# Optimization experiments

Measured on AMD Instinct MI355X. Metric: run time of the kernel, lower is better.

The kernel has to match this reference:

```python
import jax, jax.numpy as jnp
import numpy as np

B, S, D, H, L, FF, V = 2, 1024, 1024, 16, 4, 2048, 32000
DK = D // H
EPS = 1e-5  # torch LayerNorm default


def _pos_enc(n, d):
    # matches torch PositionalEncoding: pe[pos, 2i]=sin, pe[pos, 2i+1]=cos
    pos = jnp.arange(n, dtype=jnp.float32)[:, None]
    div = jnp.exp(jnp.arange(0, d, 2, dtype=jnp.float32) * (-jnp.log(10000.0) / d))
    pe = jnp.zeros((n, d), dtype=jnp.float32)
    pe = pe.at[:, 0::2].set(jnp.sin(pos * div))
    pe = pe.at[:, 1::2].set(jnp.cos(pos * div))
    return pe


def setup_inputs() -> dict:
    key = jax.random.key(0)
    ks = jax.random.split(key, 12)
    s = 0.02
    return {
        "tokens": jax.random.randint(ks[0], (B, S), 0, V, dtype=jnp.int32),
        "emb": jax.random.normal(ks[1], (V, D), jnp.float32) * s,
        "Wq": jax.random.normal(ks[2], (L, D, D), jnp.float32) * s,
        "bq": jnp.zeros((L, D), jnp.float32),
        "Wk": jax.random.normal(ks[3], (L, D, D), jnp.float32) * s,
        "bk": jnp.zeros((L, D), jnp.float32),
        "Wv": jax.random.normal(ks[4], (L, D, D), jnp.float32) * s,
        "bv": jnp.zeros((L, D), jnp.float32),
        "Wo": jax.random.normal(ks[5], (L, D, D), jnp.float32) * s,
        "bo": jnp.zeros((L, D), jnp.float32),
        "W1": jax.random.normal(ks[6], (L, D, FF), jnp.float32) * s,
        "b1": jnp.zeros((L, FF), jnp.float32),
        "W2": jax.random.normal(ks[7], (L, FF, D), jnp.float32) * s,
        "b2": jnp.zeros((L, D), jnp.float32),
        "gamma": jnp.ones((L, D), jnp.float32),
        "beta": jnp.zeros((L, D), jnp.float32),
    }


def _layernorm(x, g, b):
    mu = jnp.mean(x, axis=-1, keepdims=True)
    var = jnp.mean(jnp.square(x - mu), axis=-1, keepdims=True)
    return (x - mu) * jax.lax.rsqrt(var + EPS) * g + b


def _encoder_layer(x, p):
    Wq, bq, Wk, bk, Wv, bv, Wo, bo, W1, b1, W2, b2, g, be = p
    # naive MHA: explicit QK^T / softmax / AV, materializing [B,H,S,S]
    q = (x @ Wq + bq).reshape(B, S, H, DK).transpose(0, 2, 1, 3)
    k = (x @ Wk + bk).reshape(B, S, H, DK).transpose(0, 2, 1, 3)
    v = (x @ Wv + bv).reshape(B, S, H, DK).transpose(0, 2, 1, 3)
    scores = jnp.einsum("bhqd,bhkd->bhqk", q, k) / jnp.sqrt(jnp.float32(DK))
    attn = jax.nn.softmax(scores, axis=-1)
    o = jnp.einsum("bhqk,bhkd->bhqd", attn, v)
    o = o.transpose(0, 2, 1, 3).reshape(B, S, D) @ Wo + bo
    # NOTE: same LayerNorm params used twice, as in the original module
    x = _layernorm(x + o, g, be)
    f = jax.nn.relu(x @ W1 + b1) @ W2 + b2
    x = _layernorm(x + f, g, be)
    return x, None


def reference(tokens, emb, Wq, bq, Wk, bk, Wv, bv, Wo, bo, W1, b1, W2, b2, gamma, beta):
    x = emb[tokens]  # [B,S,D]
    # faithful to the original bug: pe[:x.size(0)] indexes the BATCH dim,
    # pe slice has shape [B,1,D] and broadcasts over the sequence dim
    x = x + _pos_enc(B, D)[:, None, :]
    params = (Wq, bq, Wk, bk, Wv, bv, Wo, bo, W1, b1, W2, b2, gamma, beta)
    x, _ = jax.lax.scan(_encoder_layer, x, params)
    return x
```

## Files before the change

### kernel.cpp

```cpp
#include <hip/hip_runtime.h>
#include <cstdint>
#include <cstddef>

#define Bx 2
#define Sx 1024
#define Dx 1024
#define Hx 16
#define Lx 4
#define FFx 2048
#define DKx 64
#define Mx (Bx * Sx)

typedef __attribute__((ext_vector_type(4))) float f32x4;
typedef __attribute__((ext_vector_type(8))) __bf16 bf16x8;

__global__ void embed_kernel(const int* __restrict__ tokens,
                             const float* __restrict__ emb,
                             float* __restrict__ x, __bf16* __restrict__ xb) {
  size_t i = (size_t)blockIdx.x * blockDim.x + threadIdx.x;
  if (i >= (size_t)Mx * Dx) return;
  int d = (int)(i % Dx);
  size_t bs = i / Dx;
  int b = (int)(bs / Sx);
  int tok = tokens[bs];
  int dd = d & ~1;
  float arg = (float)b * expf((float)dd * (-logf(10000.0f) / (float)Dx));
  float pe = (d & 1) ? cosf(arg) : sinf(arg);
  float v = emb[(size_t)tok * Dx + d] + pe;
  x[i] = v;
  xb[i] = (__bf16)v;
}

__global__ void transpose_to_bf16(const float* __restrict__ W, __bf16* __restrict__ Wt,
                                  int K, int N, size_t sstride, size_t dstride) {
  __shared__ float tile[32][33];
  const float* Ws = W + blockIdx.z * sstride;
  __bf16* Wd = Wt + blockIdx.z * dstride;
  int tx = threadIdx.x, ty = threadIdx.y;
  int n0 = blockIdx.x * 32, k0 = blockIdx.y * 32;
#pragma unroll
  for (int i = 0; i < 4; ++i)
    tile[ty + 8 * i][tx] = Ws[(size_t)(k0 + ty + 8 * i) * N + n0 + tx];
  __syncthreads();
#pragma unroll
  for (int i = 0; i < 4; ++i)
    Wd[(size_t)(n0 + ty + 8 * i) * K + k0 + tx] = (__bf16)tile[tx][ty + 8 * i];
}

__global__ void concat3_kernel(const float* __restrict__ a, const float* __restrict__ b,
                               const float* __restrict__ c, float* __restrict__ out) {
  int i = blockIdx.x * 256 + threadIdx.x;
  int l = i / 3072, j = i % 3072;
  float v = (j < 1024) ? a[l * 1024 + j]
                       : ((j < 2048) ? b[l * 1024 + j - 1024] : c[l * 1024 + j - 2048]);
  out[i] = v;
}

__global__ void transpose_v(const __bf16* __restrict__ qkvb, __bf16* __restrict__ Vt) {
  __shared__ __bf16 tile[32][40];
  int s0 = blockIdx.x * 32;
  int d0 = (blockIdx.y & 1) * 32;
  int h = blockIdx.y >> 1, b = blockIdx.z;
  int tx = threadIdx.x, ty = threadIdx.y;
  const __bf16* src = qkvb + ((size_t)b * Sx + s0) * 3072 + 2048 + h * 64 + d0;
#pragma unroll
  for (int i = 0; i < 4; ++i)
    tile[ty + 8 * i][tx] = src[(size_t)(ty + 8 * i) * 3072 + tx];
  __syncthreads();
  __bf16* dst = Vt + ((size_t)(b * Hx + h) * 64 + d0) * Sx + s0;
#pragma unroll
  for (int i = 0; i < 4; ++i)
    dst[(size_t)(ty + 8 * i) * Sx + tx] = tile[tx][ty + 8 * i];
}

__device__ __forceinline__ void gld_lds16(const void* g, void* l) {
  __builtin_amdgcn_global_load_lds(
      (const __attribute__((address_space(1))) void*)(uintptr_t)g,
      (__attribute__((address_space(3))) void*)(uintptr_t)l, 16, 0, 0);
}

template <int TM, int TN, bool RELU, typename OutT>
__global__ __launch_bounds__(256) void gemm_bt(const __bf16* __restrict__ A,
                                               const __bf16* __restrict__ Bt,
                                               const float* __restrict__ bias,
                                               OutT* __restrict__ C0,
                                               float* __restrict__ C1,
                                               int Kstep, int Kld, int ldc) {
  static_assert((TM + TN) == 192, "NCH fixed at 12");
  __shared__ __align__(16) __bf16 lds[(TM + TN) * 32];
  const int t = threadIdx.x;
  const int w = t >> 6, lane = t & 63;
  const int quad = lane >> 4, l16 = lane & 15;
  const int m0 = blockIdx.y * TM, n0 = blockIdx.x * TN;
  const int lr = lane >> 2, lc = (lane & 3) * 8;
  const int koff = blockIdx.z * Kstep;

  f32x4 acc[2][4] = {};

  const int WR = (TN == 128) ? (w >> 1) * (TM / 2) : w * (TM / 4);
  const int WC = (TN == 128) ? (w & 1) * 64 : 0;
  const __bf16* Abase = A + (size_t)m0 * Kld + koff;
  const __bf16* Bbase = Bt + (size_t)n0 * Kld + koff;

  for (int k0 = 0; k0 < Kstep; k0 += 32) {
    __syncthreads();
#pragma unroll
    for (int c = 0; c < 3; ++c) {
      const int ch = c * 4 + w;
      const int r = ch * 16 + lr;
      const __bf16* g = (r < TM) ? (Abase + (size_t)r * Kld + k0 + lc)
                                 : (Bbase + (size_t)(r - TM) * Kld + k0 + lc);
      gld_lds16(g, (void*)(lds + ch * 512));
    }
    __syncthreads();
    bf16x8 af[2], bfr[4];
#pragma unroll
    for (int i = 0; i < 2; ++i)
      af[i] = *(const bf16x8*)&lds[(WR + i * 16 + l16) * 32 + quad * 8];
#pragma unroll
    for (int j = 0; j < 4; ++j)
      bfr[j] = *(const bf16x8*)&lds[(TM + WC + j * 16 + l16) * 32 + quad * 8];
#pragma unroll
    for (int i = 0; i < 2; ++i)
#pragma unroll
      for (int j = 0; j < 4; ++j)
        acc[i][j] = __builtin_amdgcn_mfma_f32_16x16x32_bf16(af[i], bfr[j], acc[i][j], 0, 0, 0);
  }

  const bool z0 = (blockIdx.z == 0);
  const int col0 = n0 + WC + l16;
#pragma unroll
  for (int j = 0; j < 4; ++j) {
    const int n = col0 + j * 16;
    const float bn = z0 ? bias[n] : 0.f;
#pragma unroll
    for (int i = 0; i < 2; ++i) {
#pragma unroll
      for (int r = 0; r < 4; ++r) {
        const int m = m0 + WR + i * 16 + quad * 4 + r;
        float v = acc[i][j][r] + bn;
        if (RELU) v = fmaxf(v, 0.f);
        if (z0)
          C0[(size_t)m * ldc + n] = (OutT)v;
        else
          C1[(size_t)m * ldc + n] = v;
      }
    }
  }
}

__global__ __launch_bounds__(256) void attention_mfma(const __bf16* __restrict__ QKV,
                                                      const __bf16* __restrict__ Vt,
                                                      __bf16* __restrict__ O) {
  __shared__ __align__(16) __bf16 Ks[2][64 * 72];
  __shared__ __align__(16) __bf16 Vs[2][64 * 72];
  __shared__ __align__(16) __bf16 Pl[64 * 72];

  const int t = threadIdx.x;
  const int w = t >> 6, lane = t & 63;
  const int quad = lane >> 4, l16 = lane & 15;
  const int q0 = blockIdx.x * 64;
  const int h = blockIdx.y, b = blockIdx.z;
  const size_t rowbase = (size_t)b * Sx;
  const int hoff = h * 64;

  const __bf16* qrow = QKV + (rowbase + q0 + w * 16 + l16) * 3072 + hoff;
  bf16x8 qf0 = *(const bf16x8*)(qrow + quad * 8);
  bf16x8 qf1 = *(const bf16x8*)(qrow + 32 + quad * 8);

  const __bf16* Kbase = QKV + rowbase * 3072 + 1024 + hoff;
  const __bf16* Vbase = Vt + (size_t)(b * Hx + h) * 64 * Sx;

  const int srow = t >> 2, sseg = t & 3;
  bf16x8 kp0, kp1, vp0, vp1;

  f32x4 oacc[4] = {};
  f32x4 lacc = {0.f, 0.f, 0.f, 0.f};
  const float cs = 0.125f * 1.44269504089f;

  {
    const __bf16* kr = Kbase + (size_t)srow * 3072 + sseg * 16;
    kp0 = *(const bf16x8*)kr;
    kp1 = *(const bf16x8*)(kr + 8);
    const __bf16* vr = Vbase + (size_t)srow * Sx + sseg * 16;
    vp0 = *(const bf16x8*)vr;
    vp1 = *(const bf16x8*)(vr + 8);
    *(bf16x8*)&Ks[0][srow * 72 + sseg * 16] = kp0;
    *(bf16x8*)&Ks[0][srow * 72 + sseg * 16 + 8] = kp1;
    *(bf16x8*)&Vs[0][srow * 72 + sseg * 16] = vp0;
    *(bf16x8*)&Vs[0][srow * 72 + sseg * 16 + 8] = vp1;
  }
  __syncthreads();

  for (int kt = 0; kt < Sx / 64; ++kt) {
    const int cur = kt & 1;
    if (kt < Sx / 64 - 1) {
      const int kn = (kt + 1) * 64;
      const __bf16* kr = Kbase + (size_t)(kn + srow) * 3072 + sseg * 16;
      kp0 = *(const bf16x8*)kr;
      kp1 = *(const bf16x8*)(kr + 8);
      const __bf16* vr = Vbase + (size_t)srow * Sx + kn + sseg * 16;
      vp0 = *(const bf16x8*)vr;
      vp1 = *(const bf16x8*)(vr + 8);
    }

    f32x4 s[4] = {};
#pragma unroll
    for (int j = 0; j < 4; ++j) {
      bf16x8 b0 = *(const bf16x8*)&Ks[cur][(j * 16 + l16) * 72 + quad * 8];
      bf16x8 b1 = *(const bf16x8*)&Ks[cur][(j * 16 + l16) * 72 + 32 + quad * 8];
      s[j] = __builtin_amdgcn_mfma_f32_16x16x32_bf16(qf0, b0, s[j], 0, 0, 0);
      s[j] = __builtin_amdgcn_mfma_f32_16x16x32_bf16(qf1, b1, s[j], 0, 0, 0);
    }

#pragma unroll
    for (int j = 0; j < 4; ++j) {
#pragma unroll
      for (int r = 0; r < 4; ++r) s[j][r] = __builtin_exp2f(s[j][r] * cs);
      lacc += s[j];
    }

#pragma unroll
    for (int r = 0; r < 4; ++r) {
      const int prow = (w * 16 + quad * 4 + r) * 72;
#pragma unroll
      for (int j = 0; j < 4; ++j) Pl[prow + j * 16 + l16] = (__bf16)s[j][r];
    }
    bf16x8 pa0 = *(const bf16x8*)&Pl[(w * 16 + l16) * 72 + quad * 8];
    bf16x8 pa1 = *(const bf16x8*)&Pl[(w * 16 + l16) * 72 + 32 + quad * 8];

#pragma unroll
    for (int j = 0; j < 4; ++j) {
      bf16x8 vb0 = *(const bf16x8*)&Vs[cur][(j * 16 + l16) * 72 + quad * 8];
      bf16x8 vb1 = *(const bf16x8*)&Vs[cur][(j * 16 + l16) * 72 + 32 + quad * 8];
      oacc[j] = __builtin_amdgcn_mfma_f32_16x16x32_bf16(pa0, vb0, oacc[j], 0, 0, 0);
      oacc[j] = __builtin_amdgcn_mfma_f32_16x16x32_bf16(pa1, vb1, oacc[j], 0, 0, 0);
    }

    if (kt < Sx / 64 - 1) {
      const int nxt = 1 - cur;
      *(bf16x8*)&Ks[nxt][srow * 72 + sseg * 16] = kp0;
      *(bf16x8*)&Ks[nxt][srow * 72 + sseg * 16 + 8] = kp1;
      *(bf16x8*)&Vs[nxt][srow * 72 + sseg * 16] = vp0;
      *(bf16x8*)&Vs[nxt][srow * 72 + sseg * 16 + 8] = vp1;
    }
    __syncthreads();
  }

#pragma unroll
  for (int r = 0; r < 4; ++r) {
    float lr = lacc[r];
    lr += __shfl_xor(lr, 1);
    lr += __shfl_xor(lr, 2);
    lr += __shfl_xor(lr, 4);
    lr += __shfl_xor(lr, 8);
    const float inv = 1.f / lr;
    const size_t orow = (rowbase + q0 + w * 16 + quad * 4 + r) * 1024 + hoff;
#pragma unroll
    for (int j = 0; j < 4; ++j) O[orow + j * 16 + l16] = (__bf16)(oacc[j][r] * inv);
  }
}

__global__ void add_ln_kernel(const float* __restrict__ x, const float* __restrict__ r0,
                              const float* __restrict__ r1,
                              const float* __restrict__ gamma, const float* __restrict__ beta,
                              float* __restrict__ out, __bf16* __restrict__ outb) {
  int row = blockIdx.x, t = threadIdx.x;
  __shared__ float red[256];
  const float* xr = x + (size_t)row * Dx;
  const float* rr0 = r0 + (size_t)row * Dx;
  const float* rr1 = r1 + (size_t)row * Dx;
  float v[4];
  float s = 0.f;
#pragma unroll
  for (int i = 0; i < 4; ++i) {
    int c = t + i * 256;
    v[i] = xr[c] + rr0[c] + rr1[c];
    s += v[i];
  }
  red[t] = s;
  __syncthreads();
  for (int off = 128; off > 0; off >>= 1) {
    if (t < off) red[t] += red[t + off];
    __syncthreads();
  }
  float mu = red[0] * (1.f / Dx);
  __syncthreads();
  float vs = 0.f;
#pragma unroll
  for (int i = 0; i < 4; ++i) {
    float d = v[i] - mu;
    vs += d * d;
  }
  red[t] = vs;
  __syncthreads();
  for (int off = 128; off > 0; off >>= 1) {
    if (t < off) red[t] += red[t + off];
    __syncthreads();
  }
  float is = rsqrtf(red[0] * (1.f / Dx) + 1e-5f);
  float* orow = out + (size_t)row * Dx;
  __bf16* brow = outb + (size_t)row * Dx;
#pragma unroll
  for (int i = 0; i < 4; ++i) {
    int c = t + i * 256;
    float y = (v[i] - mu) * is * gamma[c] + beta[c];
    orow[c] = y;
    brow[c] = (__bf16)y;
  }
}

extern "C" void kernel_launch(void* const* d_in, const int* in_sizes, int n_in,
                              void* d_out, int out_size, void* d_ws, size_t ws_size,
                              hipStream_t stream) {
  const int* tokens = (const int*)d_in[0];
  const float* emb = (const float*)d_in[1];
  const float* Wq = (const float*)d_in[2];
  const float* bq = (const float*)d_in[3];
  const float* Wk = (const float*)d_in[4];
  const float* bk = (const float*)d_in[5];
  const float* Wv = (const float*)d_in[6];
  const float* bv = (const float*)d_in[7];
  const float* Wo = (const float*)d_in[8];
  const float* bo = (const float*)d_in[9];
  const float* W1 = (const float*)d_in[10];
  const float* b1 = (const float*)d_in[11];
  const float* W2 = (const float*)d_in[12];
  const float* b2 = (const float*)d_in[13];
  const float* gamma = (const float*)d_in[14];
  const float* beta = (const float*)d_in[15];

  const size_t M1 = 1024 * 1024;
  float* ws = (float*)d_ws;
  float* x = ws;
  float* tmp = ws + 2 * M1;
  __bf16* bfr = (__bf16*)(ws + 4 * M1);
  __bf16* xb = bfr;
  __bf16* qkvb = bfr + 2 * M1;
  __bf16* ob = bfr + 8 * M1;
  __bf16* h1b = bfr + 10 * M1;
  __bf16* Vt = bfr + 14 * M1;
  __bf16* WqkvT = bfr + 16 * M1;
  __bf16* WoT = bfr + 28 * M1;
  __bf16* W1T = bfr + 32 * M1;
  __bf16* W2T = bfr + 40 * M1;
  float* bqkv = (float*)(bfr + 48 * M1);
  float* tmp1 = (float*)qkvb;

  embed_kernel<<<((size_t)Mx * Dx + 255) / 256, 256, 0, stream>>>(tokens, emb, x, xb);

  dim3 tb(32, 8);
  transpose_to_bf16<<<dim3(32, 32, Lx), tb, 0, stream>>>(Wq, WqkvT, Dx, Dx, M1, 3 * M1);
  transpose_to_bf16<<<dim3(32, 32, Lx), tb, 0, stream>>>(Wk, WqkvT + M1, Dx, Dx, M1, 3 * M1);
  transpose_to_bf16<<<dim3(32, 32, Lx), tb, 0, stream>>>(Wv, WqkvT + 2 * M1, Dx, Dx, M1, 3 * M1);
  transpose_to_bf16<<<dim3(32, 32, Lx), tb, 0, stream>>>(Wo, WoT, Dx, Dx, M1, M1);
  transpose_to_bf16<<<dim3(64, 32, Lx), tb, 0, stream>>>(W1, W1T, Dx, FFx, 2 * M1, 2 * M1);
  transpose_to_bf16<<<dim3(32, 64, Lx), tb, 0, stream>>>(W2, W2T, FFx, Dx, 2 * M1, 2 * M1);
  concat3_kernel<<<Lx * 12, 256, 0, stream>>>(bq, bk, bv, bqkv);

  for (int l = 0; l < Lx; ++l) {
    const __bf16* WqkvT_l = WqkvT + (size_t)l * 3 * M1;
    const __bf16* WoT_l = WoT + (size_t)l * M1;
    const __bf16* W1T_l = W1T + (size_t)l * 2 * M1;
    const __bf16* W2T_l = W2T + (size_t)l * 2 * M1;
    const float* bqkv_l = bqkv + (size_t)l * 3072;
    const float* bo_l = bo + (size_t)l * Dx;
    const float* b1_l = b1 + (size_t)l * FFx;
    const float* b2_l = b2 + (size_t)l * Dx;
    const float* g_l = gamma + (size_t)l * Dx;
    const float* be_l = beta + (size_t)l * Dx;

    gemm_bt<128, 64, false, __bf16><<<dim3(3072 / 64, Mx / 128, 1), 256, 0, stream>>>(
        xb, WqkvT_l, bqkv_l, qkvb, nullptr, Dx, Dx, 3072);

    transpose_v<<<dim3(32, 32, Bx), tb, 0, stream>>>(qkvb, Vt);
    attention_mfma<<<dim3(Sx / 64, Hx, Bx), 256, 0, stream>>>(qkvb, Vt, ob);

    gemm_bt<64, 128, false, float><<<dim3(Dx / 128, Mx / 64, 2), 256, 0, stream>>>(
        ob, WoT_l, bo_l, tmp, tmp1, Dx / 2, Dx, Dx);
    add_ln_kernel<<<Mx, 256, 0, stream>>>(x, tmp, tmp1, g_l, be_l, x, xb);

    gemm_bt<128, 64, true, __bf16><<<dim3(FFx / 64, Mx / 128, 1), 256, 0, stream>>>(
        xb, W1T_l, b1_l, h1b, nullptr, Dx, Dx, FFx);
    gemm_bt<64, 128, false, float><<<dim3(Dx / 128, Mx / 64, 2), 256, 0, stream>>>(
        h1b, W2T_l, b2_l, tmp, tmp1, FFx / 2, FFx, Dx);
    add_ln_kernel<<<Mx, 256, 0, stream>>>(x, tmp, tmp1, g_l, be_l,
                                          (l == Lx - 1) ? (float*)d_out : x, xb);
  }
}
```

Before: 821.1 us.

## Fuse V transpose into QKV GEMM epilogue and vectorize LayerNorm and embedding

The QKV GEMM epilogue now writes the V columns straight into the transposed Vt layout, so the separate transpose_v kernel and its extra read and write of V are gone. The add+LayerNorm kernel is rewritten to use float4 vector loads and stores with wavefront shuffle reductions in place of a shared-memory tree that needed many barriers. The embedding kernel handles element pairs with one sincos call and float2 accesses. The V epilogue now does narrower, strided bf16x4 stores and skips writing V into qkvb, which relies on attention reading V only from Vt.

```diff
diff --git a/kernel.cpp b/kernel.cpp
--- a/kernel.cpp
+++ b/kernel.cpp
@@ -13,22 +13,30 @@
 
 typedef __attribute__((ext_vector_type(4))) float f32x4;
 typedef __attribute__((ext_vector_type(8))) __bf16 bf16x8;
+typedef __attribute__((ext_vector_type(4))) __bf16 bf16x4;
+typedef __attribute__((ext_vector_type(2))) __bf16 bf16x2;
 
 __global__ void embed_kernel(const int* __restrict__ tokens,
                              const float* __restrict__ emb,
                              float* __restrict__ x, __bf16* __restrict__ xb) {
   size_t i = (size_t)blockIdx.x * blockDim.x + threadIdx.x;
-  if (i >= (size_t)Mx * Dx) return;
-  int d = (int)(i % Dx);
-  size_t bs = i / Dx;
-  int b = (int)(bs / Sx);
+  if (i >= (size_t)Mx * Dx / 2) return;
+  int p = (int)(i % (Dx / 2));
+  size_t bs = i / (Dx / 2);
+  int b = (int)(bs >> 10);
   int tok = tokens[bs];
-  int dd = d & ~1;
-  float arg = (float)b * expf((float)dd * (-logf(10000.0f) / (float)Dx));
-  float pe = (d & 1) ? cosf(arg) : sinf(arg);
-  float v = emb[(size_t)tok * Dx + d] + pe;
-  x[i] = v;
-  xb[i] = (__bf16)v;
+  float arg = (float)b * expf((float)(2 * p) * (-logf(10000.0f) / (float)Dx));
+  float sv, cv;
+  __sincosf(arg, &sv, &cv);
+  const float2 e = ((const float2*)(emb + (size_t)tok * Dx))[p];
+  float2 o;
+  o.x = e.x + sv;
+  o.y = e.y + cv;
+  ((float2*)x)[i] = o;
+  bf16x2 ob;
+  ob[0] = (__bf16)o.x;
+  ob[1] = (__bf16)o.y;
+  ((bf16x2*)xb)[i] = ob;
 }
 
 __global__ void transpose_to_bf16(const float* __restrict__ W, __bf16* __restrict__ Wt,
@@ -56,35 +64,19 @@
   out[i] = v;
 }
 
-__global__ void transpose_v(const __bf16* __restrict__ qkvb, __bf16* __restrict__ Vt) {
-  __shared__ __bf16 tile[32][40];
-  int s0 = blockIdx.x * 32;
-  int d0 = (blockIdx.y & 1) * 32;
-  int h = blockIdx.y >> 1, b = blockIdx.z;
-  int tx = threadIdx.x, ty = threadIdx.y;
-  const __bf16* src = qkvb + ((size_t)b * Sx + s0) * 3072 + 2048 + h * 64 + d0;
-#pragma unroll
-  for (int i = 0; i < 4; ++i)
-    tile[ty + 8 * i][tx] = src[(size_t)(ty + 8 * i) * 3072 + tx];
-  __syncthreads();
-  __bf16* dst = Vt + ((size_t)(b * Hx + h) * 64 + d0) * Sx + s0;
-#pragma unroll
-  for (int i = 0; i < 4; ++i)
-    dst[(size_t)(ty + 8 * i) * Sx + tx] = tile[tx][ty + 8 * i];
-}
-
 __device__ __forceinline__ void gld_lds16(const void* g, void* l) {
   __builtin_amdgcn_global_load_lds(
       (const __attribute__((address_space(1))) void*)(uintptr_t)g,
       (__attribute__((address_space(3))) void*)(uintptr_t)l, 16, 0, 0);
 }
 
-template <int TM, int TN, bool RELU, typename OutT>
+template <int TM, int TN, bool RELU, typename OutT, bool VOUT = false>
 __global__ __launch_bounds__(256) void gemm_bt(const __bf16* __restrict__ A,
                                                const __bf16* __restrict__ Bt,
                                                const float* __restrict__ bias,
                                                OutT* __restrict__ C0,
                                                float* __restrict__ C1,
+                                               __bf16* __restrict__ VT,
                                                int Kstep, int Kld, int ldc) {
   static_assert((TM + TN) == 192, "NCH fixed at 12");
   __shared__ __align__(16) __bf16 lds[(TM + TN) * 32];
@@ -127,8 +119,29 @@
         acc[i][j] = __builtin_amdgcn_mfma_f32_16x16x32_bf16(af[i], bfr[j], acc[i][j], 0, 0, 0);
   }
 
+  const int col0 = n0 + WC + l16;
+
+  if (VOUT && n0 >= 2048) {
+    const int b = m0 >> 10;
+    const int sbase = (m0 & 1023) + WR;
+#pragma unroll
+    for (int j = 0; j < 4; ++j) {
+      const int n = col0 + j * 16;
+      const int dk = n - 2048;
+      const float bn = bias[n];
+      __bf16* vrow = VT + (size_t)(b * 1024 + dk) * Sx + sbase;
+#pragma unroll
+      for (int i = 0; i < 2; ++i) {
+        bf16x4 pk;
+#pragma unroll
+        for (int r = 0; r < 4; ++r) pk[r] = (__bf16)(acc[i][j][r] + bn);
+        *(bf16x4*)(vrow + i * 16 + quad * 4) = pk;
+      }
+    }
+    return;
+  }
+
   const bool z0 = (blockIdx.z == 0);
-  const int col0 = n0 + WC + l16;
 #pragma unroll
   for (int j = 0; j < 4; ++j) {
     const int n = col0 + j * 16;
@@ -265,49 +278,34 @@
                               const float* __restrict__ r1,
                               const float* __restrict__ gamma, const float* __restrict__ beta,
                               float* __restrict__ out, __bf16* __restrict__ outb) {
-  int row = blockIdx.x, t = threadIdx.x;
-  __shared__ float red[256];
-  const float* xr = x + (size_t)row * Dx;
-  const float* rr0 = r0 + (size_t)row * Dx;
-  const float* rr1 = r1 + (size_t)row * Dx;
-  float v[4];
-  float s = 0.f;
-#pragma unroll
-  for (int i = 0; i < 4; ++i) {
-    int c = t + i * 256;
-    v[i] = xr[c] + rr0[c] + rr1[c];
-    s += v[i];
-  }
-  red[t] = s;
+  const int row = blockIdx.x, t = threadIdx.x;
+  const int lane = t & 63, w = t >> 6;
+  __shared__ float red[2][4];
+  const f32x4* xr = (const f32x4*)(x + (size_t)row * Dx);
+  const f32x4* a0 = (const f32x4*)(r0 + (size_t)row * Dx);
+  const f32x4* a1 = (const f32x4*)(r1 + (size_t)row * Dx);
+  f32x4 v = xr[t] + a0[t] + a1[t];
+  float s = v[0] + v[1] + v[2] + v[3];
+#pragma unroll
+  for (int off = 1; off < 64; off <<= 1) s += __shfl_xor(s, off);
+  if (lane == 0) red[0][w] = s;
   __syncthreads();
-  for (int off = 128; off > 0; off >>= 1) {
-    if (t < off) red[t] += red[t + off];
-    __syncthreads();
-  }
-  float mu = red[0] * (1.f / Dx);
+  const float mu = (red[0][0] + red[0][1] + red[0][2] + red[0][3]) * (1.f / Dx);
+  f32x4 d = v - mu;
+  float vs = d[0] * d[0] + d[1] * d[1] + d[2] * d[2] + d[3] * d[3];
+#pragma unroll
+  for (int off = 1; off < 64; off <<= 1) vs += __shfl_xor(vs, off);
+  if (lane == 0) red[1][w] = vs;
   __syncthreads();
-  float vs = 0.f;
-#pragma unroll
-  for (int i = 0; i < 4; ++i) {
-    float d = v[i] - mu;
-    vs += d * d;
-  }
-  red[t] = vs;
-  __syncthreads();
-  for (int off = 128; off > 0; off >>= 1) {
-    if (t < off) red[t] += red[t + off];
-    __syncthreads();
-  }
-  float is = rsqrtf(red[0] * (1.f / Dx) + 1e-5f);
-  float* orow = out + (size_t)row * Dx;
-  __bf16* brow = outb + (size_t)row * Dx;
-#pragma unroll
-  for (int i = 0; i < 4; ++i) {
-    int c = t + i * 256;
-    float y = (v[i] - mu) * is * gamma[c] + beta[c];
-    orow[c] = y;
-    brow[c] = (__bf16)y;
-  }
+  const float is = rsqrtf((red[1][0] + red[1][1] + red[1][2] + red[1][3]) * (1.f / Dx) + 1e-5f);
+  f32x4 g = ((const f32x4*)gamma)[t];
+  f32x4 be = ((const f32x4*)beta)[t];
+  f32x4 y = d * is * g + be;
+  ((f32x4*)(out + (size_t)row * Dx))[t] = y;
+  bf16x4 yb;
+#pragma unroll
+  for (int r = 0; r < 4; ++r) yb[r] = (__bf16)y[r];
+  ((bf16x4*)(outb + (size_t)row * Dx))[t] = yb;
 }
 
 extern "C" void kernel_launch(void* const* d_in, const int* in_sizes, int n_in,
@@ -347,7 +345,7 @@
   float* bqkv = (float*)(bfr + 48 * M1);
   float* tmp1 = (float*)qkvb;
 
-  embed_kernel<<<((size_t)Mx * Dx + 255) / 256, 256, 0, stream>>>(tokens, emb, x, xb);
+  embed_kernel<<<((size_t)Mx * Dx / 2 + 255) / 256, 256, 0, stream>>>(tokens, emb, x, xb);
 
   dim3 tb(32, 8);
   transpose_to_bf16<<<dim3(32, 32, Lx), tb, 0, stream>>>(Wq, WqkvT, Dx, Dx, M1, 3 * M1);
@@ -370,20 +368,19 @@
     const float* g_l = gamma + (size_t)l * Dx;
     const float* be_l = beta + (size_t)l * Dx;
 
-    gemm_bt<128, 64, false, __bf16><<<dim3(3072 / 64, Mx / 128, 1), 256, 0, stream>>>(
-        xb, WqkvT_l, bqkv_l, qkvb, nullptr, Dx, Dx, 3072);
-
-    transpose_v<<<dim3(32, 32, Bx), tb, 0, stream>>>(qkvb, Vt);
+    gemm_bt<128, 64, false, __bf16, true><<<dim3(3072 / 64, Mx / 128, 1), 256, 0, stream>>>(
+        xb, WqkvT_l, bqkv_l, qkvb, nullptr, Vt, Dx, Dx, 3072);
+
     attention_mfma<<<dim3(Sx / 64, Hx, Bx), 256, 0, stream>>>(qkvb, Vt, ob);
 
     gemm_bt<64, 128, false, float><<<dim3(Dx / 128, Mx / 64, 2), 256, 0, stream>>>(
-        ob, WoT_l, bo_l, tmp, tmp1, Dx / 2, Dx, Dx);
+        ob, WoT_l, bo_l, tmp, tmp1, nullptr, Dx / 2, Dx, Dx);
     add_ln_kernel<<<Mx, 256, 0, stream>>>(x, tmp, tmp1, g_l, be_l, x, xb);
 
     gemm_bt<128, 64, true, __bf16><<<dim3(FFx / 64, Mx / 128, 1), 256, 0, stream>>>(
-        xb, W1T_l, b1_l, h1b, nullptr, Dx, Dx, FFx);
+        xb, W1T_l, b1_l, h1b, nullptr, nullptr, Dx, Dx, FFx);
     gemm_bt<64, 128, false, float><<<dim3(Dx / 128, Mx / 64, 2), 256, 0, stream>>>(
-        h1b, W2T_l, b2_l, tmp, tmp1, FFx / 2, FFx, Dx);
+        h1b, W2T_l, b2_l, tmp, tmp1, nullptr, FFx / 2, FFx, Dx);
     add_ln_kernel<<<Mx, 256, 0, stream>>>(x, tmp, tmp1, g_l, be_l,
                                           (l == Lx - 1) ? (float*)d_out : x, xb);
   }
```

New measurement: 806.0 us. About the same (-1.8%).
